# Kernel tuning notes

Measured on AMD Instinct MI355X. Metric: run time of the kernel, lower is better.

The kernel has to match this reference:

```python
import jax, jax.numpy as jnp
import numpy as np

N = 25000
E = 400000
IN_DIM = 512
H = 8
D = 64
ALPHA = 0.2  # leaky relu negative slope


def setup_inputs() -> dict:
    key = jax.random.key(0)
    k1, k2, k3, k4, k5 = jax.random.split(key, 5)
    inputs = jax.random.normal(k1, (N, IN_DIM), dtype=jnp.float32)
    src = jax.random.randint(k2, (E,), 0, N)
    dst = jnp.arange(E) % N  # every node has E/N inbound edges -> normalizer > 0
    # parameters (xavier-normal-ish scale)
    W = jax.random.normal(k3, (H * D, IN_DIM), dtype=jnp.float32) * (1.414 * (2.0 / (IN_DIM + H * D)) ** 0.5)
    attn_l = jax.random.normal(k4, (H, D), dtype=jnp.float32) * (1.414 * (2.0 / (D + 1)) ** 0.5)
    attn_r = jax.random.normal(k5, (H, D), dtype=jnp.float32) * (1.414 * (2.0 / (D + 1)) ** 0.5)
    return {"inputs": inputs, "W": W, "attn_l": attn_l, "attn_r": attn_r, "src": src, "dst": dst}


def reference(inputs, W, attn_l, attn_r, src, dst):
    # node projection: [N, H, D]
    ft = (inputs @ W.T).reshape(N, H, D)
    # per-node attention scalars per head: [N, H]
    a1 = jnp.einsum('nhd,hd->nh', ft, attn_l)
    a2 = jnp.einsum('nhd,hd->nh', ft, attn_r)
    # edge scores with leaky relu: [E, H]
    e = a1[src] + a2[dst]
    e = jnp.where(e > 0, e, ALPHA * e)
    # numerically stable edge softmax over incoming edges of each dst node
    emax = jax.ops.segment_max(e, dst, num_segments=N)  # [N, H]
    scores = jnp.exp(e - emax[dst])                      # [E, H]
    z = jax.ops.segment_sum(scores, dst, num_segments=N)  # [N, H]
    # weighted scatter-sum aggregation: [N, H, D]
    msg = ft[src] * scores[:, :, None]                   # [E, H, D]
    agg = jax.ops.segment_sum(msg, dst, num_segments=N)
    return agg / z[:, :, None]
```

## Files before the change

kernel.cpp:

```cpp
#include <hip/hip_runtime.h>
#include <math.h>

#define N_NODES 25000
#define E_EDGES 400000
#define IN_DIM  512
#define H_HEADS 8
#define D_HEAD  64
#define OUT_DIM 512
#define ALPHA   0.2f
#define EPN     16

typedef __attribute__((ext_vector_type(8))) short short8;
typedef __attribute__((ext_vector_type(4))) float floatx4;

__device__ __forceinline__ unsigned short f2bf(float x) {
    unsigned u = __float_as_uint(x);
    u += 0x7fffu + ((u >> 16) & 1u);
    return (unsigned short)(u >> 16);
}

__device__ __forceinline__ void gl_lds16(const unsigned short* g, unsigned short* l) {
    __builtin_amdgcn_global_load_lds((const __attribute__((address_space(1))) unsigned int*)g,
                                     (__attribute__((address_space(3))) unsigned int*)l,
                                     16, 0, 0);
}

#define A8 (N_NODES * IN_DIM / 8)
#define W8 (OUT_DIM * IN_DIM / 8)

__global__ __launch_bounds__(256) void cvt_kernel(const float* __restrict__ A,
                                                  const float* __restrict__ W,
                                                  unsigned short* __restrict__ Abf,
                                                  unsigned short* __restrict__ Wbf) {
    int idx = blockIdx.x * 256 + threadIdx.x;
    const float* s;
    unsigned short* d;
    if (idx < A8) {
        s = A + (size_t)idx * 8;
        d = Abf + (size_t)idx * 8;
    } else if (idx < A8 + W8) {
        int j = idx - A8;
        s = W + (size_t)j * 8;
        d = Wbf + (size_t)j * 8;
    } else {
        return;
    }
    float4 v0 = ((const float4*)s)[0], v1 = ((const float4*)s)[1];
    short8 o;
    o[0] = f2bf(v0.x); o[1] = f2bf(v0.y); o[2] = f2bf(v0.z); o[3] = f2bf(v0.w);
    o[4] = f2bf(v1.x); o[5] = f2bf(v1.y); o[6] = f2bf(v1.z); o[7] = f2bf(v1.w);
    *(short8*)d = o;
}

#define GBM 64
#define GBK 32

__global__ __launch_bounds__(512) void gemm_bf(const unsigned short* Abf,
                                               const unsigned short* __restrict__ Wbf,
                                               const float* __restrict__ attn_l,
                                               const float* __restrict__ attn_r,
                                               unsigned short* ftb,
                                               float* __restrict__ a1g,
                                               float* __restrict__ a2g) {
    __shared__ unsigned short As[GBM * GBK];
    __shared__ unsigned short Bs[OUT_DIM * GBK];

    const int t = threadIdx.x;
    const int wave = t >> 6;
    const int lane = t & 63;
    const int lr = lane & 15;
    const int lq = lane >> 4;
    const int mb = blockIdx.x * GBM;

    const int srow = lane >> 2;
    const int schunk = (lane & 3) * 8;
    const unsigned short* gA = Abf + (size_t)(mb + wave * 16 + srow) * IN_DIM + schunk;
    unsigned short* lA = As + wave * 16 * GBK;
    const unsigned short* gB = Wbf + (size_t)(wave * 64 + srow) * IN_DIM + schunk;
    unsigned short* lB = Bs + wave * 64 * GBK;

    floatx4 acc[4][4] = {};
    const unsigned short* a_rd = As + lr * GBK + lq * 8;
    const unsigned short* b_rd = Bs + (wave * 64 + lr) * GBK + lq * 8;

    for (int k0 = 0; k0 < IN_DIM; k0 += GBK) {
        #pragma unroll
        for (int s = 0; s < 4; ++s)
            gl_lds16(gB + (size_t)s * 16 * IN_DIM + k0, lB + s * 16 * GBK);
        if (wave < 4)
            gl_lds16(gA + k0, lA);
        __syncthreads();

        short8 af[4], bf[4];
        #pragma unroll
        for (int i = 0; i < 4; ++i) af[i] = *(const short8*)(a_rd + i * 16 * GBK);
        #pragma unroll
        for (int j = 0; j < 4; ++j) bf[j] = *(const short8*)(b_rd + j * 16 * GBK);
        #pragma unroll
        for (int i = 0; i < 4; ++i)
            #pragma unroll
            for (int j = 0; j < 4; ++j)
                acc[i][j] = __builtin_amdgcn_mfma_f32_16x16x32_bf16(af[i], bf[j], acc[i][j], 0, 0, 0);
        __syncthreads();
    }

    const int h = wave;
    float al[4], ar[4];
    #pragma unroll
    for (int j = 0; j < 4; ++j) {
        al[j] = attn_l[h * D_HEAD + j * 16 + lr];
        ar[j] = attn_r[h * D_HEAD + j * 16 + lr];
    }
    #pragma unroll
    for (int i = 0; i < 4; ++i) {
        #pragma unroll
        for (int r = 0; r < 4; ++r) {
            float s1 = 0.f, s2 = 0.f;
            #pragma unroll
            for (int j = 0; j < 4; ++j) {
                s1 += acc[i][j][r] * al[j];
                s2 += acc[i][j][r] * ar[j];
            }
            #pragma unroll
            for (int off = 1; off < 16; off <<= 1) {
                s1 += __shfl_xor(s1, off, 64);
                s2 += __shfl_xor(s2, off, 64);
            }
            if (lr == 0) {
                int n = mb + i * 16 + lq * 4 + r;
                if (n < N_NODES) {
                    a1g[h * N_NODES + n] = s1;
                    a2g[h * N_NODES + n] = s2;
                }
            }
        }
    }

    #pragma unroll
    for (int i = 0; i < 4; ++i) {
        #pragma unroll
        for (int j = 0; j < 4; ++j) {
            const int nrow = mb + i * 16 + lq * 4;
            const int col = wave * 64 + j * 16 + lr;
            #pragma unroll
            for (int r = 0; r < 4; ++r) {
                int nn = nrow + r;
                if (nn < N_NODES)
                    ftb[(size_t)nn * OUT_DIM + col] = f2bf(acc[i][j][r]);
            }
        }
    }
}

__global__ __launch_bounds__(256, 3) void agg_kernel(const unsigned short* __restrict__ ftb,
                                                     const float* __restrict__ a1T,
                                                     const float* __restrict__ a2T,
                                                     const int* __restrict__ src,
                                                     float* __restrict__ out) {
    __shared__ float s_w[32][EPN + 1];
    __shared__ int   s_is[32][EPN + 1];

    const int h     = blockIdx.x & 7;
    const int chunk = blockIdx.x >> 3;
    const int t = threadIdx.x;
    const int nd = t >> 3;
    const int l  = t & 7;
    const int v  = chunk * 32 + nd;
    const bool valid = v < N_NODES;
    const int vc = valid ? v : N_NODES - 1;

    {
        int s0 = src[vc + l * N_NODES];
        int s1 = src[vc + (l + 8) * N_NODES];
        float a2v = a2T[h * N_NODES + vc];
        float x0 = a1T[h * N_NODES + s0] + a2v;
        float x1 = a1T[h * N_NODES + s1] + a2v;
        float e0 = x0 > 0.f ? x0 : ALPHA * x0;
        float e1 = x1 > 0.f ? x1 : ALPHA * x1;
        float m = fmaxf(e0, e1);
        #pragma unroll
        for (int off = 1; off < 8; off <<= 1) m = fmaxf(m, __shfl_xor(m, off, 64));
        float w0 = __expf(e0 - m), w1 = __expf(e1 - m);
        float z = w0 + w1;
        #pragma unroll
        for (int off = 1; off < 8; off <<= 1) z += __shfl_xor(z, off, 64);
        float iz = 1.f / z;
        s_w[nd][l]      = w0 * iz;
        s_w[nd][l + 8]  = w1 * iz;
        s_is[nd][l]     = s0;
        s_is[nd][l + 8] = s1;
    }
    __syncthreads();

    float wl[EPN];
    const unsigned short* ap[EPN];
    const unsigned short* fp = ftb + h * D_HEAD + l * 8;
    #pragma unroll
    for (int j = 0; j < EPN; ++j) {
        wl[j] = s_w[nd][j];
        ap[j] = fp + (size_t)s_is[nd][j] * OUT_DIM;
    }
    uint4 q[EPN];
    #pragma unroll
    for (int j = 0; j < EPN; ++j) q[j] = *(const uint4*)ap[j];

    float acc[8] = {};
    #pragma unroll
    for (int j = 0; j < EPN; ++j) {
        float wj = wl[j];
        acc[0] += wj * __uint_as_float(q[j].x << 16);
        acc[1] += wj * __uint_as_float(q[j].x & 0xffff0000u);
        acc[2] += wj * __uint_as_float(q[j].y << 16);
        acc[3] += wj * __uint_as_float(q[j].y & 0xffff0000u);
        acc[4] += wj * __uint_as_float(q[j].z << 16);
        acc[5] += wj * __uint_as_float(q[j].z & 0xffff0000u);
        acc[6] += wj * __uint_as_float(q[j].w << 16);
        acc[7] += wj * __uint_as_float(q[j].w & 0xffff0000u);
    }
    if (valid) {
        floatx4* op = (floatx4*)(out + (size_t)v * OUT_DIM + h * D_HEAD + l * 8);
        floatx4 o0 = {acc[0], acc[1], acc[2], acc[3]};
        floatx4 o1 = {acc[4], acc[5], acc[6], acc[7]};
        __builtin_nontemporal_store(o0, op + 0);
        __builtin_nontemporal_store(o1, op + 1);
    }
}

extern "C" void kernel_launch(void* const* d_in, const int* in_sizes, int n_in,
                              void* d_out, int out_size, void* d_ws, size_t ws_size,
                              hipStream_t stream) {
    const float* inputs = (const float*)d_in[0];
    const float* W      = (const float*)d_in[1];
    const float* attn_l = (const float*)d_in[2];
    const float* attn_r = (const float*)d_in[3];
    const int*   src    = (const int*)d_in[4];

    float* out = (float*)d_out;
    unsigned short* buf0 = (unsigned short*)d_ws;
    unsigned short* Wbf  = buf0 + (size_t)N_NODES * IN_DIM;
    float* a1 = (float*)(Wbf + (size_t)OUT_DIM * IN_DIM);
    float* a2 = a1 + (size_t)N_NODES * H_HEADS;

    cvt_kernel<<<(A8 + W8 + 255) / 256, 256, 0, stream>>>(inputs, W, buf0, Wbf);

    gemm_bf<<<(N_NODES + GBM - 1) / GBM, 512, 0, stream>>>(buf0, Wbf, attn_l, attn_r,
                                                           buf0, a1, a2);

    agg_kernel<<<8 * ((N_NODES + 31) / 32), 256, 0, stream>>>(buf0, a1, a2, src, out);
}
```

Measured before the change: 169.1 us.

## Fuse input fp32-to-bf16 conversion into GEMM and double-buffer LDS tiles

The separate pass that converted the whole input matrix to bf16 is removed. The GEMM now loads fp32 input rows directly, converts them in registers and writes them to LDS, so the bf16 copy of the activations is never written to or read back from global memory. The shared-memory tiles for both operands are double-buffered so the next k-step's loads overlap with the current MFMAs. This doubles LDS use and puts the conversion work inside the GEMM, which could lower occupancy.

```diff
diff --git a/kernel.cpp b/kernel.cpp
--- a/kernel.cpp
+++ b/kernel.cpp
@@ -11,6 +11,7 @@
 #define EPN     16
 
 typedef __attribute__((ext_vector_type(8))) short short8;
+typedef __attribute__((ext_vector_type(4))) short short4v;
 typedef __attribute__((ext_vector_type(4))) float floatx4;
 
 __device__ __forceinline__ unsigned short f2bf(float x) {
@@ -25,45 +26,33 @@
                                      16, 0, 0);
 }
 
-#define A8 (N_NODES * IN_DIM / 8)
 #define W8 (OUT_DIM * IN_DIM / 8)
 
-__global__ __launch_bounds__(256) void cvt_kernel(const float* __restrict__ A,
-                                                  const float* __restrict__ W,
-                                                  unsigned short* __restrict__ Abf,
-                                                  unsigned short* __restrict__ Wbf) {
+__global__ __launch_bounds__(256) void cvt_w(const float* __restrict__ W,
+                                             unsigned short* __restrict__ Wbf) {
     int idx = blockIdx.x * 256 + threadIdx.x;
-    const float* s;
-    unsigned short* d;
-    if (idx < A8) {
-        s = A + (size_t)idx * 8;
-        d = Abf + (size_t)idx * 8;
-    } else if (idx < A8 + W8) {
-        int j = idx - A8;
-        s = W + (size_t)j * 8;
-        d = Wbf + (size_t)j * 8;
-    } else {
-        return;
-    }
+    if (idx >= W8) return;
+    const float* s = W + (size_t)idx * 8;
     float4 v0 = ((const float4*)s)[0], v1 = ((const float4*)s)[1];
     short8 o;
     o[0] = f2bf(v0.x); o[1] = f2bf(v0.y); o[2] = f2bf(v0.z); o[3] = f2bf(v0.w);
     o[4] = f2bf(v1.x); o[5] = f2bf(v1.y); o[6] = f2bf(v1.z); o[7] = f2bf(v1.w);
-    *(short8*)d = o;
+    *(short8*)(Wbf + (size_t)idx * 8) = o;
 }
 
 #define GBM 64
 #define GBK 32
-
-__global__ __launch_bounds__(512) void gemm_bf(const unsigned short* Abf,
+#define NKSTEP (IN_DIM / GBK)
+
+__global__ __launch_bounds__(512) void gemm_bf(const float* __restrict__ A,
                                                const unsigned short* __restrict__ Wbf,
                                                const float* __restrict__ attn_l,
                                                const float* __restrict__ attn_r,
-                                               unsigned short* ftb,
+                                               unsigned short* __restrict__ ftb,
                                                float* __restrict__ a1g,
                                                float* __restrict__ a2g) {
-    __shared__ unsigned short As[GBM * GBK];
-    __shared__ unsigned short Bs[OUT_DIM * GBK];
+    __shared__ unsigned short As[2][GBM * GBK];
+    __shared__ unsigned short Bs[2][OUT_DIM * GBK];
 
     const int t = threadIdx.x;
     const int wave = t >> 6;
@@ -74,34 +63,63 @@
 
     const int srow = lane >> 2;
     const int schunk = (lane & 3) * 8;
-    const unsigned short* gA = Abf + (size_t)(mb + wave * 16 + srow) * IN_DIM + schunk;
-    unsigned short* lA = As + wave * 16 * GBK;
     const unsigned short* gB = Wbf + (size_t)(wave * 64 + srow) * IN_DIM + schunk;
-    unsigned short* lB = Bs + wave * 64 * GBK;
+
+    const int arow = t >> 3;
+    const int acol = (t & 7) * 4;
+    int ar_g = mb + arow;
+    if (ar_g >= N_NODES) ar_g = N_NODES - 1;
+    const float* gA = A + (size_t)ar_g * IN_DIM + acol;
+    const int a_off = arow * GBK + acol;
 
     floatx4 acc[4][4] = {};
-    const unsigned short* a_rd = As + lr * GBK + lq * 8;
-    const unsigned short* b_rd = Bs + (wave * 64 + lr) * GBK + lq * 8;
-
-    for (int k0 = 0; k0 < IN_DIM; k0 += GBK) {
+
+    {
         #pragma unroll
         for (int s = 0; s < 4; ++s)
-            gl_lds16(gB + (size_t)s * 16 * IN_DIM + k0, lB + s * 16 * GBK);
-        if (wave < 4)
-            gl_lds16(gA + k0, lA);
+            gl_lds16(gB + (size_t)s * 16 * IN_DIM, &Bs[0][wave * 64 * GBK + s * 16 * GBK]);
+        floatx4 av = __builtin_nontemporal_load((const floatx4*)gA);
+        short4v o;
+        o[0] = f2bf(av[0]); o[1] = f2bf(av[1]); o[2] = f2bf(av[2]); o[3] = f2bf(av[3]);
+        *(short4v*)&As[0][a_off] = o;
+    }
+    __syncthreads();
+
+    int cur = 0;
+    for (int ks = 0; ks < NKSTEP; ++ks) {
+        const int nxt = cur ^ 1;
+        const bool more = (ks + 1 < NKSTEP);
+        const int k1 = (ks + 1) * GBK;
+
+        floatx4 av;
+        if (more) {
+            #pragma unroll
+            for (int s = 0; s < 4; ++s)
+                gl_lds16(gB + (size_t)s * 16 * IN_DIM + k1,
+                         &Bs[nxt][wave * 64 * GBK + s * 16 * GBK]);
+            av = __builtin_nontemporal_load((const floatx4*)(gA + k1));
+        }
+
+        const unsigned short* a_rd = &As[cur][lr * GBK + lq * 8];
+        const unsigned short* b_rd = &Bs[cur][(wave * 64 + lr) * GBK + lq * 8];
+        short8 af[4], bq[4];
+        #pragma unroll
+        for (int i = 0; i < 4; ++i) af[i] = *(const short8*)(a_rd + i * 16 * GBK);
+        #pragma unroll
+        for (int j = 0; j < 4; ++j) bq[j] = *(const short8*)(b_rd + j * 16 * GBK);
+        #pragma unroll
+        for (int i = 0; i < 4; ++i)
+            #pragma unroll
+            for (int j = 0; j < 4; ++j)
+                acc[i][j] = __builtin_amdgcn_mfma_f32_16x16x32_bf16(af[i], bq[j], acc[i][j], 0, 0, 0);
+
+        if (more) {
+            short4v o;
+            o[0] = f2bf(av[0]); o[1] = f2bf(av[1]); o[2] = f2bf(av[2]); o[3] = f2bf(av[3]);
+            *(short4v*)&As[nxt][a_off] = o;
+        }
         __syncthreads();
-
-        short8 af[4], bf[4];
-        #pragma unroll
-        for (int i = 0; i < 4; ++i) af[i] = *(const short8*)(a_rd + i * 16 * GBK);
-        #pragma unroll
-        for (int j = 0; j < 4; ++j) bf[j] = *(const short8*)(b_rd + j * 16 * GBK);
-        #pragma unroll
-        for (int i = 0; i < 4; ++i)
-            #pragma unroll
-            for (int j = 0; j < 4; ++j)
-                acc[i][j] = __builtin_amdgcn_mfma_f32_16x16x32_bf16(af[i], bf[j], acc[i][j], 0, 0, 0);
-        __syncthreads();
+        cur = nxt;
     }
 
     const int h = wave;
@@ -236,15 +254,15 @@
     const int*   src    = (const int*)d_in[4];
 
     float* out = (float*)d_out;
-    unsigned short* buf0 = (unsigned short*)d_ws;
-    unsigned short* Wbf  = buf0 + (size_t)N_NODES * IN_DIM;
+    unsigned short* ftb = (unsigned short*)d_ws;
+    unsigned short* Wbf = ftb + (size_t)N_NODES * IN_DIM;
     float* a1 = (float*)(Wbf + (size_t)OUT_DIM * IN_DIM);
     float* a2 = a1 + (size_t)N_NODES * H_HEADS;
 
-    cvt_kernel<<<(A8 + W8 + 255) / 256, 256, 0, stream>>>(inputs, W, buf0, Wbf);
-
-    gemm_bf<<<(N_NODES + GBM - 1) / GBM, 512, 0, stream>>>(buf0, Wbf, attn_l, attn_r,
-                                                           buf0, a1, a2);
-
-    agg_kernel<<<8 * ((N_NODES + 31) / 32), 256, 0, stream>>>(buf0, a1, a2, src, out);
-}
+    cvt_w<<<(W8 + 255) / 256, 256, 0, stream>>>(W, Wbf);
+
+    gemm_bf<<<(N_NODES + GBM - 1) / GBM, 512, 0, stream>>>(inputs, Wbf, attn_l, attn_r,
+                                                           ftb, a1, a2);
+
+    agg_kernel<<<8 * ((N_NODES + 31) / 32), 256, 0, stream>>>(ftb, a1, a2, src, out);
+}
```

Result: slower. 186.7 us (+10.4%).

## Double-buffer LDS tiles in projection GEMM to overlap loads with MFMA

Applied to the files above, without the earlier changes.

Splits the A and B shared-memory tiles into two buffers. The global-to-LDS loads for the next K step are issued before the MFMA work on the current buffer, and the loop now uses one barrier per step instead of two. The aim is to hide global load latency behind matrix math. In exchange, LDS use per block doubles (about 72KB), which can reduce occupancy. Correctness depends on the barrier also covering completion of the async LDS loads.

```diff
diff --git a/kernel.cpp b/kernel.cpp
--- a/kernel.cpp
+++ b/kernel.cpp
@@ -54,6 +54,7 @@
 
 #define GBM 64
 #define GBK 32
+#define NKSTEP (IN_DIM / GBK)
 
 __global__ __launch_bounds__(512) void gemm_bf(const unsigned short* Abf,
                                                const unsigned short* __restrict__ Wbf,
@@ -62,8 +63,8 @@
                                                unsigned short* ftb,
                                                float* __restrict__ a1g,
                                                float* __restrict__ a2g) {
-    __shared__ unsigned short As[GBM * GBK];
-    __shared__ unsigned short Bs[OUT_DIM * GBK];
+    __shared__ unsigned short As[2][GBM * GBK];
+    __shared__ unsigned short Bs[2][OUT_DIM * GBK];
 
     const int t = threadIdx.x;
     const int wave = t >> 6;
@@ -75,33 +76,48 @@
     const int srow = lane >> 2;
     const int schunk = (lane & 3) * 8;
     const unsigned short* gA = Abf + (size_t)(mb + wave * 16 + srow) * IN_DIM + schunk;
-    unsigned short* lA = As + wave * 16 * GBK;
     const unsigned short* gB = Wbf + (size_t)(wave * 64 + srow) * IN_DIM + schunk;
-    unsigned short* lB = Bs + wave * 64 * GBK;
 
     floatx4 acc[4][4] = {};
-    const unsigned short* a_rd = As + lr * GBK + lq * 8;
-    const unsigned short* b_rd = Bs + (wave * 64 + lr) * GBK + lq * 8;
-
-    for (int k0 = 0; k0 < IN_DIM; k0 += GBK) {
+
+    {
         #pragma unroll
         for (int s = 0; s < 4; ++s)
-            gl_lds16(gB + (size_t)s * 16 * IN_DIM + k0, lB + s * 16 * GBK);
+            gl_lds16(gB + (size_t)s * 16 * IN_DIM, &Bs[0][wave * 64 * GBK + s * 16 * GBK]);
         if (wave < 4)
-            gl_lds16(gA + k0, lA);
+            gl_lds16(gA, &As[0][wave * 16 * GBK]);
+    }
+    __syncthreads();
+
+    int cur = 0;
+    for (int ks = 0; ks < NKSTEP; ++ks) {
+        const int nxt = cur ^ 1;
+        const int k1 = (ks + 1) * GBK;
+
+        if (ks + 1 < NKSTEP) {
+            #pragma unroll
+            for (int s = 0; s < 4; ++s)
+                gl_lds16(gB + (size_t)s * 16 * IN_DIM + k1,
+                         &Bs[nxt][wave * 64 * GBK + s * 16 * GBK]);
+            if (wave < 4)
+                gl_lds16(gA + k1, &As[nxt][wave * 16 * GBK]);
+        }
+
+        const unsigned short* a_rd = &As[cur][lr * GBK + lq * 8];
+        const unsigned short* b_rd = &Bs[cur][(wave * 64 + lr) * GBK + lq * 8];
+        short8 af[4], bq[4];
+        #pragma unroll
+        for (int i = 0; i < 4; ++i) af[i] = *(const short8*)(a_rd + i * 16 * GBK);
+        #pragma unroll
+        for (int j = 0; j < 4; ++j) bq[j] = *(const short8*)(b_rd + j * 16 * GBK);
+        #pragma unroll
+        for (int i = 0; i < 4; ++i)
+            #pragma unroll
+            for (int j = 0; j < 4; ++j)
+                acc[i][j] = __builtin_amdgcn_mfma_f32_16x16x32_bf16(af[i], bq[j], acc[i][j], 0, 0, 0);
+
         __syncthreads();
-
-        short8 af[4], bf[4];
-        #pragma unroll
-        for (int i = 0; i < 4; ++i) af[i] = *(const short8*)(a_rd + i * 16 * GBK);
-        #pragma unroll
-        for (int j = 0; j < 4; ++j) bf[j] = *(const short8*)(b_rd + j * 16 * GBK);
-        #pragma unroll
-        for (int i = 0; i < 4; ++i)
-            #pragma unroll
-            for (int j = 0; j < 4; ++j)
-                acc[i][j] = __builtin_amdgcn_mfma_f32_16x16x32_bf16(af[i], bf[j], acc[i][j], 0, 0, 0);
-        __syncthreads();
+        cur = nxt;
     }
 
     const int h = wave;
```

Result: slower. 180.5 us (+6.8%).

## Retile projection GEMM into 128x128 output tiles with separate ft buffer

Applied to the files above, without the earlier changes.

The projection GEMM changes from 64-row blocks that each cover all 512 output columns with 8 waves to 128x128 tiles with 4 waves in a 2x2 arrangement, so each block streams a 128-row slice of W instead of all of it. This reduces W traffic per output and cuts shared memory per block, which lets more blocks run per CU and spreads work over about 4x as many blocks. The bf16 projection output now goes to its own workspace buffer instead of overwriting the converted input in place. That in-place write was only safe when one block owned whole rows, and it is unsafe now that four column blocks read the same rows. The cost is extra workspace and the A tile being reloaded by four column blocks.

```diff
diff --git a/kernel.cpp b/kernel.cpp
--- a/kernel.cpp
+++ b/kernel.cpp
@@ -52,59 +52,67 @@
     *(short8*)d = o;
 }
 
-#define GBM 64
+#define TBM 128
+#define TBN 128
 #define GBK 32
-
-__global__ __launch_bounds__(512) void gemm_bf(const unsigned short* Abf,
+#define NCB (OUT_DIM / TBN)
+#define NRB ((N_NODES + TBM - 1) / TBM)
+
+__global__ __launch_bounds__(256) void gemm_bf(const unsigned short* __restrict__ Abf,
                                                const unsigned short* __restrict__ Wbf,
                                                const float* __restrict__ attn_l,
                                                const float* __restrict__ attn_r,
-                                               unsigned short* ftb,
+                                               unsigned short* __restrict__ ftb,
                                                float* __restrict__ a1g,
                                                float* __restrict__ a2g) {
-    __shared__ unsigned short As[GBM * GBK];
-    __shared__ unsigned short Bs[OUT_DIM * GBK];
+    __shared__ unsigned short As[TBM * GBK];
+    __shared__ unsigned short Bs[TBN * GBK];
 
     const int t = threadIdx.x;
-    const int wave = t >> 6;
+    const int w = t >> 6;
     const int lane = t & 63;
     const int lr = lane & 15;
     const int lq = lane >> 4;
-    const int mb = blockIdx.x * GBM;
+    const int wr = w >> 1;
+    const int wc = w & 1;
+
+    const int cb = blockIdx.x & (NCB - 1);
+    const int rb = blockIdx.x >> 2;
+    const int mb = rb * TBM;
 
     const int srow = lane >> 2;
     const int schunk = (lane & 3) * 8;
-    const unsigned short* gA = Abf + (size_t)(mb + wave * 16 + srow) * IN_DIM + schunk;
-    unsigned short* lA = As + wave * 16 * GBK;
-    const unsigned short* gB = Wbf + (size_t)(wave * 64 + srow) * IN_DIM + schunk;
-    unsigned short* lB = Bs + wave * 64 * GBK;
+    const unsigned short* gA = Abf + (size_t)(mb + w * 16 + srow) * IN_DIM + schunk;
+    const unsigned short* gB = Wbf + (size_t)(cb * TBN + w * 16 + srow) * IN_DIM + schunk;
+    unsigned short* lA = As + w * 512;
+    unsigned short* lB = Bs + w * 512;
 
     floatx4 acc[4][4] = {};
-    const unsigned short* a_rd = As + lr * GBK + lq * 8;
-    const unsigned short* b_rd = Bs + (wave * 64 + lr) * GBK + lq * 8;
+    const unsigned short* a_rd = As + (wr * 64 + lr) * GBK + lq * 8;
+    const unsigned short* b_rd = Bs + (wc * 64 + lr) * GBK + lq * 8;
 
     for (int k0 = 0; k0 < IN_DIM; k0 += GBK) {
         #pragma unroll
-        for (int s = 0; s < 4; ++s)
-            gl_lds16(gB + (size_t)s * 16 * IN_DIM + k0, lB + s * 16 * GBK);
-        if (wave < 4)
-            gl_lds16(gA + k0, lA);
+        for (int s = 0; s < 2; ++s) {
+            gl_lds16(gA + (size_t)s * 64 * IN_DIM + k0, lA + s * 2048);
+            gl_lds16(gB + (size_t)s * 64 * IN_DIM + k0, lB + s * 2048);
+        }
         __syncthreads();
 
-        short8 af[4], bf[4];
+        short8 af[4], bq[4];
         #pragma unroll
         for (int i = 0; i < 4; ++i) af[i] = *(const short8*)(a_rd + i * 16 * GBK);
         #pragma unroll
-        for (int j = 0; j < 4; ++j) bf[j] = *(const short8*)(b_rd + j * 16 * GBK);
+        for (int j = 0; j < 4; ++j) bq[j] = *(const short8*)(b_rd + j * 16 * GBK);
         #pragma unroll
         for (int i = 0; i < 4; ++i)
             #pragma unroll
             for (int j = 0; j < 4; ++j)
-                acc[i][j] = __builtin_amdgcn_mfma_f32_16x16x32_bf16(af[i], bf[j], acc[i][j], 0, 0, 0);
+                acc[i][j] = __builtin_amdgcn_mfma_f32_16x16x32_bf16(af[i], bq[j], acc[i][j], 0, 0, 0);
         __syncthreads();
     }
 
-    const int h = wave;
+    const int h = cb * 2 + wc;
     float al[4], ar[4];
     #pragma unroll
     for (int j = 0; j < 4; ++j) {
@@ -127,7 +135,7 @@
                 s2 += __shfl_xor(s2, off, 64);
             }
             if (lr == 0) {
-                int n = mb + i * 16 + lq * 4 + r;
+                int n = mb + wr * 64 + i * 16 + lq * 4 + r;
                 if (n < N_NODES) {
                     a1g[h * N_NODES + n] = s1;
                     a2g[h * N_NODES + n] = s2;
@@ -140,8 +148,8 @@
     for (int i = 0; i < 4; ++i) {
         #pragma unroll
         for (int j = 0; j < 4; ++j) {
-            const int nrow = mb + i * 16 + lq * 4;
-            const int col = wave * 64 + j * 16 + lr;
+            const int nrow = mb + wr * 64 + i * 16 + lq * 4;
+            const int col = cb * TBN + wc * 64 + j * 16 + lr;
             #pragma unroll
             for (int r = 0; r < 4; ++r) {
                 int nn = nrow + r;
@@ -236,15 +244,15 @@
     const int*   src    = (const int*)d_in[4];
 
     float* out = (float*)d_out;
-    unsigned short* buf0 = (unsigned short*)d_ws;
-    unsigned short* Wbf  = buf0 + (size_t)N_NODES * IN_DIM;
+    unsigned short* Abf = (unsigned short*)d_ws;
+    unsigned short* Wbf = Abf + (size_t)N_NODES * IN_DIM;
     float* a1 = (float*)(Wbf + (size_t)OUT_DIM * IN_DIM);
     float* a2 = a1 + (size_t)N_NODES * H_HEADS;
-
-    cvt_kernel<<<(A8 + W8 + 255) / 256, 256, 0, stream>>>(inputs, W, buf0, Wbf);
-
-    gemm_bf<<<(N_NODES + GBM - 1) / GBM, 512, 0, stream>>>(buf0, Wbf, attn_l, attn_r,
-                                                           buf0, a1, a2);
-
-    agg_kernel<<<8 * ((N_NODES + 31) / 32), 256, 0, stream>>>(buf0, a1, a2, src, out);
-}
+    unsigned short* ftb = (unsigned short*)(a2 + (size_t)N_NODES * H_HEADS);
+
+    cvt_kernel<<<(A8 + W8 + 255) / 256, 256, 0, stream>>>(inputs, W, Abf, Wbf);
+
+    gemm_bf<<<NRB * NCB, 256, 0, stream>>>(Abf, Wbf, attn_l, attn_r, ftb, a1, a2);
+
+    agg_kernel<<<8 * ((N_NODES + 31) / 32), 256, 0, stream>>>(ftb, a1, a2, src, out);
+}
```

After: 173.7 us. +2.7%, slower.
